# Performance work log

Hardware: AMD Instinct MI355X
Metric: run time of the kernel (lower is better)

The kernel has to match this reference:

```python
import jax, jax.numpy as jnp
import numpy as np

N = 100_000          # nodes
E = 3_200_000        # edges (avg degree 32)
IN = 128             # input feature dim
H = 4                # heads
D = 16               # out feats per head
NEG_SLOPE = 0.2


def setup_inputs() -> dict:
    key = jax.random.key(0)
    ks = jax.random.split(key, 7)
    h = jax.random.normal(ks[0], (N, IN), dtype=jnp.float32)
    W = jax.random.normal(ks[1], (H * D, IN), dtype=jnp.float32) * (1.0 / np.sqrt(IN))
    attn_l = jax.random.normal(ks[2], (H, D), dtype=jnp.float32) * 0.1
    attn_r = jax.random.normal(ks[3], (H, D), dtype=jnp.float32) * 0.1
    bias = jax.random.normal(ks[4], (H * D,), dtype=jnp.float32) * 0.01
    src = jax.random.randint(ks[5], (E,), 0, N, dtype=jnp.int32)
    dst = jax.random.randint(ks[6], (E,), 0, N, dtype=jnp.int32)
    return {"h": h, "W": W, "attn_l": attn_l, "attn_r": attn_r,
            "bias": bias, "src": src, "dst": dst}


def reference(h, W, attn_l, attn_r, bias, src, dst):
    # Linear projection: [N, IN] @ [IN, H*D] -> [N, H, D]
    feat = (h @ W.T).reshape(N, H, D)
    # Per-node attention logits (a_l^T Wh_src, a_r^T Wh_dst): [N, H]
    el = jnp.einsum('nhd,hd->nh', feat, attn_l)
    er = jnp.einsum('nhd,hd->nh', feat, attn_r)
    # Edge scores with LeakyReLU: [E, H]
    e = el[src] + er[dst]
    e = jnp.where(e > 0, e, NEG_SLOPE * e)
    # Segment softmax over incoming edges of each destination node
    m = jax.ops.segment_max(e, dst, num_segments=N)          # [N, H]
    m = jnp.where(jnp.isfinite(m), m, 0.0)                   # empty segments
    ex = jnp.exp(e - m[dst])                                 # [E, H]
    s = jax.ops.segment_sum(ex, dst, num_segments=N)         # [N, H]
    alpha = ex / jnp.where(s[dst] > 0, s[dst], 1.0)          # [E, H]
    # Weighted scatter-sum aggregation: [E, H, D] messages -> [N, H, D]
    msg = feat[src] * alpha[:, :, None]
    out = jax.ops.segment_sum(msg, dst, num_segments=N)
    out = out + bias.reshape(1, H, D)
    return out
```

## Files before the change

kernel.cpp:

```cpp
#include <hip/hip_runtime.h>

#define N_NODES 100000
#define N_EDGES 3200000
#define IN_DIM  128
#define HEADS   4
#define OUT_DIM 64
#define NEG_SLOPE 0.2f

#define BSH   9
#define BNOD  (1 << BSH)
#define BMSK  (BNOD - 1)
#define NBUCK 196
#define MAXB  19456
#define CHUNK 8192
#define NCHUNK 391
#define BPAD  16

typedef __attribute__((ext_vector_type(8))) short bf16x8;
typedef __attribute__((ext_vector_type(4))) float f32x4;

__device__ inline unsigned short f2bf_rne(float x) {
    unsigned u = __float_as_uint(x);
    u += 0x7FFFu + ((u >> 16) & 1u);
    return (unsigned short)(u >> 16);
}
__device__ inline float wsum64(float v) {
    #pragma unroll
    for (int o = 32; o; o >>= 1) v += __shfl_xor(v, o);
    return v;
}

__global__ __launch_bounds__(256) void gat_prep(
    const float* __restrict__ W, unsigned short* __restrict__ Whi,
    unsigned short* __restrict__ Wlo, int* __restrict__ bcur)
{
    const int i = blockIdx.x * 256 + threadIdx.x;
    if (i < NBUCK) bcur[i * BPAD] = i * MAXB;
    if (i < OUT_DIM * IN_DIM) {
        const float w = W[i];
        const unsigned short hi = f2bf_rne(w);
        const float whif = __uint_as_float((unsigned)hi << 16);
        Whi[i] = hi;
        Wlo[i] = f2bf_rne(w - whif);
    }
}

__global__ __launch_bounds__(256) void gat_gemm(
    const float* __restrict__ h,
    const unsigned short* __restrict__ Whi, const unsigned short* __restrict__ Wlo,
    const float* __restrict__ attn_l, const float* __restrict__ attn_r,
    unsigned short* __restrict__ featbf, float* __restrict__ el, float* __restrict__ er)
{
    const int tid  = threadIdx.x;
    const int w    = tid >> 6;
    const int lane = tid & 63;
    const int row  = lane & 15;
    const int kg   = lane >> 4;
    const int n0   = blockIdx.x * 64 + w * 16;

    int gn = n0 + row; if (gn >= N_NODES) gn = N_NODES - 1;
    const float* hrow = h + (size_t)gn * IN_DIM;

    bf16x8 ahi[4], alo[4];
    #pragma unroll
    for (int kc = 0; kc < 4; ++kc) {
        const float4 f0 = *reinterpret_cast<const float4*>(hrow + kc * 32 + kg * 8);
        const float4 f1 = *reinterpret_cast<const float4*>(hrow + kc * 32 + kg * 8 + 4);
        const float f[8] = {f0.x, f0.y, f0.z, f0.w, f1.x, f1.y, f1.z, f1.w};
        #pragma unroll
        for (int j = 0; j < 8; ++j) {
            const unsigned short hi = f2bf_rne(f[j]);
            const float hif = __uint_as_float((unsigned)hi << 16);
            ahi[kc][j] = (short)hi;
            alo[kc][j] = (short)f2bf_rne(f[j] - hif);
        }
    }

    f32x4 acc[4];
    #pragma unroll
    for (int ob = 0; ob < 4; ++ob) acc[ob] = (f32x4){0.f, 0.f, 0.f, 0.f};

    #pragma unroll
    for (int kc = 0; kc < 4; ++kc) {
        #pragma unroll
        for (int ob = 0; ob < 4; ++ob) {
            const size_t woff = (size_t)(ob * 16 + row) * IN_DIM + kc * 32 + kg * 8;
            const bf16x8 bhi = *reinterpret_cast<const bf16x8*>(Whi + woff);
            const bf16x8 blo = *reinterpret_cast<const bf16x8*>(Wlo + woff);
            acc[ob] = __builtin_amdgcn_mfma_f32_16x16x32_bf16(ahi[kc], bhi, acc[ob], 0, 0, 0);
            acc[ob] = __builtin_amdgcn_mfma_f32_16x16x32_bf16(ahi[kc], blo, acc[ob], 0, 0, 0);
            acc[ob] = __builtin_amdgcn_mfma_f32_16x16x32_bf16(alo[kc], bhi, acc[ob], 0, 0, 0);
        }
    }

    float alv[4], arv[4];
    #pragma unroll
    for (int ob = 0; ob < 4; ++ob) {
        alv[ob] = attn_l[ob * 16 + row];
        arv[ob] = attn_r[ob * 16 + row];
    }
    #pragma unroll
    for (int ob = 0; ob < 4; ++ob) {
        #pragma unroll
        for (int reg = 0; reg < 4; ++reg) {
            const int node = n0 + kg * 4 + reg;
            float vl = acc[ob][reg] * alv[ob];
            float vr = acc[ob][reg] * arv[ob];
            #pragma unroll
            for (int off = 1; off < 16; off <<= 1) {
                vl += __shfl_xor(vl, off);
                vr += __shfl_xor(vr, off);
            }
            if (row == 0 && node < N_NODES) {
                el[node * 4 + ob] = vl;
                er[node * 4 + ob] = vr;
            }
            const unsigned bfv = (unsigned)f2bf_rne(acc[ob][reg]);
            const unsigned pw = (unsigned)__shfl_xor((int)bfv, 1);
            if (!(lane & 1) && node < N_NODES) {
                *reinterpret_cast<unsigned*>(featbf + (size_t)node * OUT_DIM + ob * 16 + row) =
                    (bfv & 0xFFFFu) | (pw << 16);
            }
        }
    }
}

__global__ __launch_bounds__(256) void gat_bin(
    const int* __restrict__ src, const int* __restrict__ dst,
    int* __restrict__ bcur, unsigned int* __restrict__ binned)
{
    __shared__ int cnt[NBUCK];
    __shared__ int boff[NBUCK];
    const int tid  = threadIdx.x;
    const int base = blockIdx.x * CHUNK;
    const int nval = min(CHUNK, N_EDGES - base);

    if (tid < NBUCK) cnt[tid] = 0;
    __syncthreads();
    for (int i = tid; i < nval; i += 256)
        atomicAdd(&cnt[dst[base + i] >> BSH], 1);
    __syncthreads();
    if (tid < NBUCK) {
        int c2 = cnt[tid];
        boff[tid] = c2 ? atomicAdd(&bcur[tid * BPAD], c2) : 0;
    }
    __syncthreads();
    for (int i = tid; i < nval; i += 256) {
        int d = dst[base + i], s = src[base + i];
        int k = d >> BSH;
        int slot = atomicAdd(&boff[k], 1);
        int lim = (k + 1) * MAXB - 1;
        if (slot > lim) slot = lim;
        binned[slot] = ((unsigned)s << BSH) | (unsigned)(d & BMSK);
    }
}

__global__ __launch_bounds__(1024) void gat_sortb(
    const unsigned int* __restrict__ binned, const int* __restrict__ bcur,
    int* __restrict__ csr, int* __restrict__ nbeg, int* __restrict__ nend)
{
    __shared__ int lhist[BNOD];
    __shared__ int lofs[BNOD];
    __shared__ int lcur[BNOD];
    const int b = blockIdx.x;
    const int tid = threadIdx.x;
    const int nodebase = b << BSH;
    const int beg = b * MAXB;
    const int end = min(bcur[b * BPAD], beg + MAXB);

    if (tid < BNOD) lhist[tid] = 0;
    __syncthreads();
    for (int i = beg + tid; i < end; i += 1024)
        atomicAdd(&lhist[binned[i] & BMSK], 1);
    __syncthreads();
    if (tid < BNOD) lofs[tid] = lhist[tid];
    __syncthreads();
    #pragma unroll
    for (int off = 1; off < BNOD; off <<= 1) {
        int t = (tid < BNOD && tid >= off) ? lofs[tid - off] : 0;
        __syncthreads();
        if (tid < BNOD) lofs[tid] += t;
        __syncthreads();
    }
    if (tid < BNOD) {
        const int v = lhist[tid];
        const int e0 = lofs[tid] - v;
        lcur[tid] = e0;
        const int n = nodebase + tid;
        if (n < N_NODES) { nbeg[n] = beg + e0; nend[n] = beg + lofs[tid]; }
    }
    __syncthreads();
    for (int i = beg + tid; i < end; i += 1024) {
        const unsigned u = binned[i];
        const int pos = atomicAdd(&lcur[u & BMSK], 1);
        csr[beg + pos] = (int)(u >> BSH);
    }
}

__global__ __launch_bounds__(256) void gat_agg(
    const int* __restrict__ nbeg, const int* __restrict__ nend,
    const int* __restrict__ csr,
    const float* __restrict__ el, const float* __restrict__ er,
    const unsigned short* __restrict__ featbf, const float* __restrict__ bias,
    float* __restrict__ out)
{
    __shared__ float pb[4][4 * 68];
    __shared__ int   sb[4][64];
    const int w = threadIdx.x >> 6;
    const int n = blockIdx.x * 4 + w;
    if (n >= N_NODES) return;
    const int lane = threadIdx.x & 63;
    const int eo = lane >> 4;
    const int cs = lane & 15;
    const int hh = cs >> 2;

    const float4 er4 = *reinterpret_cast<const float4*>(er + n * 4);
    const float4 b4  = *reinterpret_cast<const float4*>(bias + 4 * cs);
    const int beg = nbeg[n], end = nend[n];

    float ss0 = 0.f, ss1 = 0.f, ss2 = 0.f, ss3 = 0.f;
    float a0 = 0.f, a1 = 0.f, a2 = 0.f, a3 = 0.f;

    for (int c = beg; c < end; c += 64) {
        const int nv = min(64, end - c);
        const bool act = lane < nv;
        const int mysrc = act ? csr[c + lane] : 0;

        const float4 el4 = *reinterpret_cast<const float4*>(el + mysrc * 4);
        float sc0 = el4.x + er4.x, sc1 = el4.y + er4.y;
        float sc2 = el4.z + er4.z, sc3 = el4.w + er4.w;
        sc0 = sc0 > 0.f ? sc0 : NEG_SLOPE * sc0;
        sc1 = sc1 > 0.f ? sc1 : NEG_SLOPE * sc1;
        sc2 = sc2 > 0.f ? sc2 : NEG_SLOPE * sc2;
        sc3 = sc3 > 0.f ? sc3 : NEG_SLOPE * sc3;
        if (!act) { sc0 = sc1 = sc2 = sc3 = -1e30f; }

        const float p0 = __expf(sc0), p1 = __expf(sc1);
        const float p2 = __expf(sc2), p3 = __expf(sc3);
        ss0 += p0; ss1 += p1; ss2 += p2; ss3 += p3;

        pb[w][0 * 68 + lane] = p0;
        pb[w][1 * 68 + lane] = p1;
        pb[w][2 * 68 + lane] = p2;
        pb[w][3 * 68 + lane] = p3;
        sb[w][lane] = mysrc;

        const int steps = (nv + 3) >> 2;
        #pragma unroll 4
        for (int j = 0; j < steps; ++j) {
            const int e4 = 4 * j + eo;
            const int s  = sb[w][e4];
            const float p = pb[w][hh * 68 + e4];
            const uint2 q = *reinterpret_cast<const uint2*>(
                featbf + (size_t)s * OUT_DIM + 4 * cs);
            a0 = fmaf(p, __uint_as_float(q.x << 16),          a0);
            a1 = fmaf(p, __uint_as_float(q.x & 0xFFFF0000u),  a1);
            a2 = fmaf(p, __uint_as_float(q.y << 16),          a2);
            a3 = fmaf(p, __uint_as_float(q.y & 0xFFFF0000u),  a3);
        }
    }

    a0 += __shfl_xor(a0, 16); a0 += __shfl_xor(a0, 32);
    a1 += __shfl_xor(a1, 16); a1 += __shfl_xor(a1, 32);
    a2 += __shfl_xor(a2, 16); a2 += __shfl_xor(a2, 32);
    a3 += __shfl_xor(a3, 16); a3 += __shfl_xor(a3, 32);

    const float t0 = wsum64(ss0), t1 = wsum64(ss1);
    const float t2 = wsum64(ss2), t3 = wsum64(ss3);
    const float sv = hh == 0 ? t0 : hh == 1 ? t1 : hh == 2 ? t2 : t3;
    const float inv = 1.f / (sv > 0.f ? sv : 1.f);

    if (eo == 0) {
        float4 o4;
        o4.x = a0 * inv + b4.x; o4.y = a1 * inv + b4.y;
        o4.z = a2 * inv + b4.z; o4.w = a3 * inv + b4.w;
        *reinterpret_cast<float4*>(out + (size_t)n * OUT_DIM + 4 * cs) = o4;
    }
}

extern "C" void kernel_launch(void* const* d_in, const int* in_sizes, int n_in,
                              void* d_out, int out_size, void* d_ws, size_t ws_size,
                              hipStream_t stream) {
    const float* h      = (const float*)d_in[0];
    const float* W      = (const float*)d_in[1];
    const float* attn_l = (const float*)d_in[2];
    const float* attn_r = (const float*)d_in[3];
    const float* bias   = (const float*)d_in[4];
    const int*   src    = (const int*)d_in[5];
    const int*   dst    = (const int*)d_in[6];
    float* out = (float*)d_out;

    unsigned short* featbf = (unsigned short*)d_ws;
    float* el   = (float*)(featbf + (size_t)N_NODES * OUT_DIM);
    float* er   = el + (size_t)N_NODES * HEADS;
    unsigned short* Whi = (unsigned short*)(er + (size_t)N_NODES * HEADS);
    unsigned short* Wlo = Whi + OUT_DIM * IN_DIM;
    int*   bcur = (int*)(Wlo + OUT_DIM * IN_DIM);
    unsigned int* binned = (unsigned int*)(bcur + NBUCK * BPAD + 16);
    int*   csr  = (int*)(binned + (size_t)NBUCK * MAXB);
    int*   nbeg = csr + (size_t)NBUCK * MAXB;
    int*   nend = nbeg + N_NODES;

    gat_prep<<<32, 256, 0, stream>>>(W, Whi, Wlo, bcur);
    gat_gemm<<<(N_NODES + 63) / 64, 256, 0, stream>>>(h, Whi, Wlo, attn_l, attn_r, featbf, el, er);
    gat_bin<<<NCHUNK, 256, 0, stream>>>(src, dst, bcur, binned);
    gat_sortb<<<NBUCK, 1024, 0, stream>>>(binned, bcur, csr, nbeg, nend);
    gat_agg<<<(N_NODES + 3) / 4, 256, 0, stream>>>(nbeg, nend, csr, el, er, featbf, bias, out);
}
```

Measured before the change: 175.4 us.

## Merge GEMM and edge binning into one launch, shuffle-scan sort, prefetch CSR

Fuses the projection GEMM and the edge-binning kernel into one launch, with disjoint block ranges, so the two independent stages can run concurrently and one launch is saved. Replaces the shared-memory Hillis-Steele prefix scan in the per-bucket sort with a wavefront shuffle scan plus a small cross-wave pass, which cuts the number of barriers. In aggregation, the next chunk of CSR source indices is loaded before the current chunk is processed, to hide that load's latency. The fused kernel carries the union of both stages' register and LDS use, which can lower occupancy for the GEMM blocks.

```diff
diff --git a/kernel.cpp b/kernel.cpp
--- a/kernel.cpp
+++ b/kernel.cpp
@@ -15,6 +15,7 @@
 #define CHUNK 8192
 #define NCHUNK 391
 #define BPAD  16
+#define NGEMMB 1563
 
 typedef __attribute__((ext_vector_type(8))) short bf16x8;
 typedef __attribute__((ext_vector_type(4))) float f32x4;
@@ -45,113 +46,112 @@
     }
 }
 
-__global__ __launch_bounds__(256) void gat_gemm(
+__global__ __launch_bounds__(256) void gat_gb(
     const float* __restrict__ h,
     const unsigned short* __restrict__ Whi, const unsigned short* __restrict__ Wlo,
     const float* __restrict__ attn_l, const float* __restrict__ attn_r,
-    unsigned short* __restrict__ featbf, float* __restrict__ el, float* __restrict__ er)
-{
-    const int tid  = threadIdx.x;
-    const int w    = tid >> 6;
-    const int lane = tid & 63;
-    const int row  = lane & 15;
-    const int kg   = lane >> 4;
-    const int n0   = blockIdx.x * 64 + w * 16;
-
-    int gn = n0 + row; if (gn >= N_NODES) gn = N_NODES - 1;
-    const float* hrow = h + (size_t)gn * IN_DIM;
-
-    bf16x8 ahi[4], alo[4];
-    #pragma unroll
-    for (int kc = 0; kc < 4; ++kc) {
-        const float4 f0 = *reinterpret_cast<const float4*>(hrow + kc * 32 + kg * 8);
-        const float4 f1 = *reinterpret_cast<const float4*>(hrow + kc * 32 + kg * 8 + 4);
-        const float f[8] = {f0.x, f0.y, f0.z, f0.w, f1.x, f1.y, f1.z, f1.w};
-        #pragma unroll
-        for (int j = 0; j < 8; ++j) {
-            const unsigned short hi = f2bf_rne(f[j]);
-            const float hif = __uint_as_float((unsigned)hi << 16);
-            ahi[kc][j] = (short)hi;
-            alo[kc][j] = (short)f2bf_rne(f[j] - hif);
-        }
-    }
-
-    f32x4 acc[4];
-    #pragma unroll
-    for (int ob = 0; ob < 4; ++ob) acc[ob] = (f32x4){0.f, 0.f, 0.f, 0.f};
-
-    #pragma unroll
-    for (int kc = 0; kc < 4; ++kc) {
-        #pragma unroll
-        for (int ob = 0; ob < 4; ++ob) {
-            const size_t woff = (size_t)(ob * 16 + row) * IN_DIM + kc * 32 + kg * 8;
-            const bf16x8 bhi = *reinterpret_cast<const bf16x8*>(Whi + woff);
-            const bf16x8 blo = *reinterpret_cast<const bf16x8*>(Wlo + woff);
-            acc[ob] = __builtin_amdgcn_mfma_f32_16x16x32_bf16(ahi[kc], bhi, acc[ob], 0, 0, 0);
-            acc[ob] = __builtin_amdgcn_mfma_f32_16x16x32_bf16(ahi[kc], blo, acc[ob], 0, 0, 0);
-            acc[ob] = __builtin_amdgcn_mfma_f32_16x16x32_bf16(alo[kc], bhi, acc[ob], 0, 0, 0);
-        }
-    }
-
-    float alv[4], arv[4];
-    #pragma unroll
-    for (int ob = 0; ob < 4; ++ob) {
-        alv[ob] = attn_l[ob * 16 + row];
-        arv[ob] = attn_r[ob * 16 + row];
-    }
-    #pragma unroll
-    for (int ob = 0; ob < 4; ++ob) {
-        #pragma unroll
-        for (int reg = 0; reg < 4; ++reg) {
-            const int node = n0 + kg * 4 + reg;
-            float vl = acc[ob][reg] * alv[ob];
-            float vr = acc[ob][reg] * arv[ob];
-            #pragma unroll
-            for (int off = 1; off < 16; off <<= 1) {
-                vl += __shfl_xor(vl, off);
-                vr += __shfl_xor(vr, off);
-            }
-            if (row == 0 && node < N_NODES) {
-                el[node * 4 + ob] = vl;
-                er[node * 4 + ob] = vr;
-            }
-            const unsigned bfv = (unsigned)f2bf_rne(acc[ob][reg]);
-            const unsigned pw = (unsigned)__shfl_xor((int)bfv, 1);
-            if (!(lane & 1) && node < N_NODES) {
-                *reinterpret_cast<unsigned*>(featbf + (size_t)node * OUT_DIM + ob * 16 + row) =
-                    (bfv & 0xFFFFu) | (pw << 16);
-            }
-        }
-    }
-}
-
-__global__ __launch_bounds__(256) void gat_bin(
+    unsigned short* __restrict__ featbf, float* __restrict__ el, float* __restrict__ er,
     const int* __restrict__ src, const int* __restrict__ dst,
     int* __restrict__ bcur, unsigned int* __restrict__ binned)
 {
     __shared__ int cnt[NBUCK];
     __shared__ int boff[NBUCK];
-    const int tid  = threadIdx.x;
-    const int base = blockIdx.x * CHUNK;
-    const int nval = min(CHUNK, N_EDGES - base);
-
-    if (tid < NBUCK) cnt[tid] = 0;
-    __syncthreads();
-    for (int i = tid; i < nval; i += 256)
-        atomicAdd(&cnt[dst[base + i] >> BSH], 1);
-    __syncthreads();
-    if (tid < NBUCK) {
-        int c2 = cnt[tid];
-        boff[tid] = c2 ? atomicAdd(&bcur[tid * BPAD], c2) : 0;
-    }
-    __syncthreads();
-    for (int i = tid; i < nval; i += 256) {
-        int d = dst[base + i], s = src[base + i];
-        int k = d >> BSH;
-        int slot = atomicAdd(&boff[k], 1);
-        int lim = (k + 1) * MAXB - 1;
-        if (slot > lim) slot = lim;
-        binned[slot] = ((unsigned)s << BSH) | (unsigned)(d & BMSK);
+    const int tid = threadIdx.x;
+
+    if (blockIdx.x < NGEMMB) {
+        const int w    = tid >> 6;
+        const int lane = tid & 63;
+        const int row  = lane & 15;
+        const int kg   = lane >> 4;
+        const int n0   = blockIdx.x * 64 + w * 16;
+
+        int gn = n0 + row; if (gn >= N_NODES) gn = N_NODES - 1;
+        const float* hrow = h + (size_t)gn * IN_DIM;
+
+        bf16x8 ahi[4], alo[4];
+        #pragma unroll
+        for (int kc = 0; kc < 4; ++kc) {
+            const float4 f0 = *reinterpret_cast<const float4*>(hrow + kc * 32 + kg * 8);
+            const float4 f1 = *reinterpret_cast<const float4*>(hrow + kc * 32 + kg * 8 + 4);
+            const float f[8] = {f0.x, f0.y, f0.z, f0.w, f1.x, f1.y, f1.z, f1.w};
+            #pragma unroll
+            for (int j = 0; j < 8; ++j) {
+                const unsigned short hi = f2bf_rne(f[j]);
+                const float hif = __uint_as_float((unsigned)hi << 16);
+                ahi[kc][j] = (short)hi;
+                alo[kc][j] = (short)f2bf_rne(f[j] - hif);
+            }
+        }
+
+        f32x4 acc[4];
+        #pragma unroll
+        for (int ob = 0; ob < 4; ++ob) acc[ob] = (f32x4){0.f, 0.f, 0.f, 0.f};
+
+        #pragma unroll
+        for (int kc = 0; kc < 4; ++kc) {
+            #pragma unroll
+            for (int ob = 0; ob < 4; ++ob) {
+                const size_t woff = (size_t)(ob * 16 + row) * IN_DIM + kc * 32 + kg * 8;
+                const bf16x8 bhi = *reinterpret_cast<const bf16x8*>(Whi + woff);
+                const bf16x8 blo = *reinterpret_cast<const bf16x8*>(Wlo + woff);
+                acc[ob] = __builtin_amdgcn_mfma_f32_16x16x32_bf16(ahi[kc], bhi, acc[ob], 0, 0, 0);
+                acc[ob] = __builtin_amdgcn_mfma_f32_16x16x32_bf16(ahi[kc], blo, acc[ob], 0, 0, 0);
+                acc[ob] = __builtin_amdgcn_mfma_f32_16x16x32_bf16(alo[kc], bhi, acc[ob], 0, 0, 0);
+            }
+        }
+
+        float alv[4], arv[4];
+        #pragma unroll
+        for (int ob = 0; ob < 4; ++ob) {
+            alv[ob] = attn_l[ob * 16 + row];
+            arv[ob] = attn_r[ob * 16 + row];
+        }
+        #pragma unroll
+        for (int ob = 0; ob < 4; ++ob) {
+            #pragma unroll
+            for (int reg = 0; reg < 4; ++reg) {
+                const int node = n0 + kg * 4 + reg;
+                float vl = acc[ob][reg] * alv[ob];
+                float vr = acc[ob][reg] * arv[ob];
+                #pragma unroll
+                for (int off = 1; off < 16; off <<= 1) {
+                    vl += __shfl_xor(vl, off);
+                    vr += __shfl_xor(vr, off);
+                }
+                if (row == 0 && node < N_NODES) {
+                    el[node * 4 + ob] = vl;
+                    er[node * 4 + ob] = vr;
+                }
+                const unsigned bfv = (unsigned)f2bf_rne(acc[ob][reg]);
+                const unsigned pw = (unsigned)__shfl_xor((int)bfv, 1);
+                if (!(lane & 1) && node < N_NODES) {
+                    *reinterpret_cast<unsigned*>(featbf + (size_t)node * OUT_DIM + ob * 16 + row) =
+                        (bfv & 0xFFFFu) | (pw << 16);
+                }
+            }
+        }
+    } else {
+        const int base = (blockIdx.x - NGEMMB) * CHUNK;
+        const int nval = min(CHUNK, N_EDGES - base);
+
+        if (tid < NBUCK) cnt[tid] = 0;
+        __syncthreads();
+        for (int i = tid; i < nval; i += 256)
+            atomicAdd(&cnt[dst[base + i] >> BSH], 1);
+        __syncthreads();
+        if (tid < NBUCK) {
+            int c2 = cnt[tid];
+            boff[tid] = c2 ? atomicAdd(&bcur[tid * BPAD], c2) : 0;
+        }
+        __syncthreads();
+        for (int i = tid; i < nval; i += 256) {
+            int d = dst[base + i], s = src[base + i];
+            int k = d >> BSH;
+            int slot = atomicAdd(&boff[k], 1);
+            int lim = (k + 1) * MAXB - 1;
+            if (slot > lim) slot = lim;
+            binned[slot] = ((unsigned)s << BSH) | (unsigned)(d & BMSK);
+        }
     }
 }
 
@@ -160,8 +160,8 @@
     int* __restrict__ csr, int* __restrict__ nbeg, int* __restrict__ nend)
 {
     __shared__ int lhist[BNOD];
-    __shared__ int lofs[BNOD];
     __shared__ int lcur[BNOD];
+    __shared__ int wtot[8];
     const int b = blockIdx.x;
     const int tid = threadIdx.x;
     const int nodebase = b << BSH;
@@ -173,21 +173,36 @@
     for (int i = beg + tid; i < end; i += 1024)
         atomicAdd(&lhist[binned[i] & BMSK], 1);
     __syncthreads();
-    if (tid < BNOD) lofs[tid] = lhist[tid];
-    __syncthreads();
-    #pragma unroll
-    for (int off = 1; off < BNOD; off <<= 1) {
-        int t = (tid < BNOD && tid >= off) ? lofs[tid - off] : 0;
-        __syncthreads();
-        if (tid < BNOD) lofs[tid] += t;
-        __syncthreads();
-    }
+
+    int v = 0, inc = 0;
     if (tid < BNOD) {
-        const int v = lhist[tid];
-        const int e0 = lofs[tid] - v;
+        v = lhist[tid];
+        inc = v;
+        #pragma unroll
+        for (int off = 1; off < 64; off <<= 1) {
+            int t = __shfl_up(inc, off, 64);
+            if ((tid & 63) >= off) inc += t;
+        }
+        if ((tid & 63) == 63) wtot[tid >> 6] = inc;
+    }
+    __syncthreads();
+    if (tid < 8) {
+        int t = wtot[tid];
+        int inc2 = t;
+        #pragma unroll
+        for (int off = 1; off < 8; off <<= 1) {
+            int u = __shfl_up(inc2, off, 64);
+            if (tid >= off) inc2 += u;
+        }
+        wtot[tid] = inc2 - t;
+    }
+    __syncthreads();
+    if (tid < BNOD) {
+        const int incl = inc + wtot[tid >> 6];
+        const int e0 = incl - v;
         lcur[tid] = e0;
         const int n = nodebase + tid;
-        if (n < N_NODES) { nbeg[n] = beg + e0; nend[n] = beg + lofs[tid]; }
+        if (n < N_NODES) { nbeg[n] = beg + e0; nend[n] = beg + incl; }
     }
     __syncthreads();
     for (int i = beg + tid; i < end; i += 1024) {
@@ -221,10 +236,13 @@
     float ss0 = 0.f, ss1 = 0.f, ss2 = 0.f, ss3 = 0.f;
     float a0 = 0.f, a1 = 0.f, a2 = 0.f, a3 = 0.f;
 
+    int mysrc = (beg + lane < end) ? csr[beg + lane] : 0;
+
     for (int c = beg; c < end; c += 64) {
         const int nv = min(64, end - c);
         const bool act = lane < nv;
-        const int mysrc = act ? csr[c + lane] : 0;
+        const int nidx = c + 64 + lane;
+        const int nxt = (nidx < end) ? csr[nidx] : 0;
 
         const float4 el4 = *reinterpret_cast<const float4*>(el + mysrc * 4);
         float sc0 = el4.x + er4.x, sc1 = el4.y + er4.y;
@@ -258,6 +276,7 @@
             a2 = fmaf(p, __uint_as_float(q.y << 16),          a2);
             a3 = fmaf(p, __uint_as_float(q.y & 0xFFFF0000u),  a3);
         }
+        mysrc = nxt;
     }
 
     a0 += __shfl_xor(a0, 16); a0 += __shfl_xor(a0, 32);
@@ -302,8 +321,8 @@
     int*   nend = nbeg + N_NODES;
 
     gat_prep<<<32, 256, 0, stream>>>(W, Whi, Wlo, bcur);
-    gat_gemm<<<(N_NODES + 63) / 64, 256, 0, stream>>>(h, Whi, Wlo, attn_l, attn_r, featbf, el, er);
-    gat_bin<<<NCHUNK, 256, 0, stream>>>(src, dst, bcur, binned);
+    gat_gb<<<NGEMMB + NCHUNK, 256, 0, stream>>>(h, Whi, Wlo, attn_l, attn_r,
+                                                featbf, el, er, src, dst, bcur, binned);
     gat_sortb<<<NBUCK, 1024, 0, stream>>>(binned, bcur, csr, nbeg, nend);
     gat_agg<<<(N_NODES + 3) / 4, 256, 0, stream>>>(nbeg, nend, csr, el, er, featbf, bias, out);
 }
```

Result: faster. 165.3 us (-5.8%).
